# Kernel optimization log

Measured on AMD Instinct MI355X. Metric: run time of the kernel, lower is better.

The kernel has to match this reference:

```python
import jax, jax.numpy as jnp
import numpy as np

H = 64        # hidden_dim
HEADS = 4
HD = H // HEADS

def setup_inputs() -> dict:
    key = jax.random.key(0)
    ks = jax.random.split(key, 32)
    def w(k, shape, fan_in):
        return jax.random.normal(k, shape, dtype=jnp.float32) * (1.0 / np.sqrt(fan_in))
    inp = {
        'robot_states': jax.random.normal(ks[0], (32, 512, 7), dtype=jnp.float32),
        'task_states': jax.random.normal(ks[1], (32, 128, 6), dtype=jnp.float32),
        # robot encoder: Linear(7,H) ReLU Linear(H,H) ReLU
        'r_w1': w(ks[2], (7, H), 7),  'r_b1': jnp.zeros((H,), jnp.float32),
        'r_w2': w(ks[3], (H, H), H),  'r_b2': jnp.zeros((H,), jnp.float32),
        # task encoder: Linear(6,H) ReLU Linear(H,H) ReLU
        't_w1': w(ks[4], (6, H), 6),  't_b1': jnp.zeros((H,), jnp.float32),
        't_w2': w(ks[5], (H, H), H),  't_b2': jnp.zeros((H,), jnp.float32),
        # MultiheadAttention (query=tasks, key/value=robots)
        'wq': w(ks[6], (H, H), H), 'bq': jnp.zeros((H,), jnp.float32),
        'wk': w(ks[7], (H, H), H), 'bk': jnp.zeros((H,), jnp.float32),
        'wv': w(ks[8], (H, H), H), 'bv': jnp.zeros((H,), jnp.float32),
        'wo': w(ks[9], (H, H), H), 'bo': jnp.zeros((H,), jnp.float32),
        # allocation net: Linear(2H,H) ReLU Linear(H,H//2) ReLU Linear(H//2,1)
        'a_w1': w(ks[10], (2 * H, H), 2 * H), 'a_b1': jnp.zeros((H,), jnp.float32),
        'a_w2': w(ks[11], (H, H // 2), H),    'a_b2': jnp.zeros((H // 2,), jnp.float32),
        'a_w3': w(ks[12], (H // 2, 1), H // 2), 'a_b3': jnp.zeros((1,), jnp.float32),
        'num_robots': 512,
        'num_tasks': 128,
    }
    return inp

def reference(robot_states, task_states, r_w1, r_b1, r_w2, r_b2,
              t_w1, t_b1, t_w2, t_b2, wq, bq, wk, bk, wv, bv, wo, bo,
              a_w1, a_b1, a_w2, a_b2, a_w3, a_b3, num_robots, num_tasks):
    relu = jax.nn.relu
    B = robot_states.shape[0]
    # encoders
    rf = relu(relu(robot_states @ r_w1 + r_b1) @ r_w2 + r_b2)[:, :num_robots]  # [B,R,H]
    tf = relu(relu(task_states @ t_w1 + t_b1) @ t_w2 + t_b2)[:, :num_tasks]    # [B,T,H]
    # multihead attention: tasks attend to robots
    q = (tf @ wq + bq).reshape(B, -1, HEADS, HD)
    k = (rf @ wk + bk).reshape(B, -1, HEADS, HD)
    v = (rf @ wv + bv).reshape(B, -1, HEADS, HD)
    logits = jnp.einsum('bthd,brhd->bhtr', q, k) / np.sqrt(HD)
    attn = jax.nn.softmax(logits, axis=-1)
    ctx = jnp.einsum('bhtr,brhd->bthd', attn, v).reshape(B, -1, H)
    tf = ctx @ wo + bo  # [B,T,H]
    # pairwise allocation MLP: concat([task, robot]) @ a_w1 split into two halves
    tp = tf @ a_w1[:H]   # [B,T,H]
    rp = rf @ a_w1[H:]   # [B,R,H]
    h1 = relu(tp[:, :, None, :] + rp[:, None, :, :] + a_b1)  # [B,T,R,H]
    h2 = relu(h1 @ a_w2 + a_b2)                              # [B,T,R,H//2]
    scores = (h2 @ a_w3)[..., 0] + a_b3[0]                   # [B,T,R]
    return jax.nn.softmax(scores, axis=-1)
```

## Files before the change

### kernel.cpp

```cpp
#include <hip/hip_runtime.h>
#include <hip/hip_bf16.h>
#include <math.h>

#define NB 32
#define NR 512
#define NT 128

typedef __attribute__((ext_vector_type(8))) short short8;
typedef __attribute__((ext_vector_type(4))) float f32x4;
typedef __attribute__((ext_vector_type(2))) float f32x2;

#define DPPF(s, ctrl) \
  __int_as_float(__builtin_amdgcn_update_dpp(0, __float_as_int(s), ctrl, 0xf, 0xf, true))

__device__ __forceinline__ float wred_max(float v){
  v = fmaxf(v, DPPF(v, 0xB1));
  v = fmaxf(v, DPPF(v, 0x4E));
  v = fmaxf(v, DPPF(v, 0x141));
  v = fmaxf(v, DPPF(v, 0x140));
  v = fmaxf(v, __shfl_xor(v, 16));
  v = fmaxf(v, __shfl_xor(v, 32));
  return v;
}
__device__ __forceinline__ float wred_sum(float v){
  v += DPPF(v, 0xB1);
  v += DPPF(v, 0x4E);
  v += DPPF(v, 0x141);
  v += DPPF(v, 0x140);
  v += __shfl_xor(v, 16);
  v += __shfl_xor(v, 32);
  return v;
}

__device__ __forceinline__ float dpp_add16(float s){
  int x;
  x = __builtin_amdgcn_update_dpp(0, __float_as_int(s), 0x111, 0xf, 0xf, true);
  s += __int_as_float(x);
  x = __builtin_amdgcn_update_dpp(0, __float_as_int(s), 0x112, 0xf, 0xf, true);
  s += __int_as_float(x);
  x = __builtin_amdgcn_update_dpp(0, __float_as_int(s), 0x114, 0xf, 0xf, true);
  s += __int_as_float(x);
  x = __builtin_amdgcn_update_dpp(0, __float_as_int(s), 0x118, 0xf, 0xf, true);
  s += __int_as_float(x);
  return s;
}

__global__ __launch_bounds__(256) void enc_kernel(
    const float* __restrict__ rs, const float* __restrict__ ts,
    const float* __restrict__ r_w1, const float* __restrict__ r_b1,
    const float* __restrict__ r_w2, const float* __restrict__ r_b2,
    const float* __restrict__ t_w1, const float* __restrict__ t_b1,
    const float* __restrict__ t_w2, const float* __restrict__ t_b2,
    const float* __restrict__ wq, const float* __restrict__ bq,
    const float* __restrict__ wk, const float* __restrict__ bk,
    const float* __restrict__ wv, const float* __restrict__ bv,
    const float* __restrict__ a_w1, const float* __restrict__ a_w2,
    float* __restrict__ kbuf, float* __restrict__ vbuf,
    float* __restrict__ rpbuf, float* __restrict__ qbuf,
    unsigned short* __restrict__ w2f)
{
  __shared__ float w1s[448];
  __shared__ float wss[4096];
  __shared__ float h_s[32 * 66];
  __shared__ float rf_s[32 * 66];

  const int tid = threadIdx.x;
  const int blk = blockIdx.x;

  if (blk == 640) {
    if (tid < 64) {
      int l = tid, n16 = l & 15, g = l >> 4;
      for (int f = 0; f < 8; ++f) {
        int ntile = f & 1, ks = (f >> 1) & 1, part = f >> 2;
        for (int j = 0; j < 8; ++j) {
          int k = ks * 32 + g * 8 + j;
          int n = ntile * 16 + n16;
          unsigned wb = __float_as_uint(a_w2[k * 32 + n]);
          unsigned hib = wb & 0xffff0000u;
          float lof = __uint_as_float(wb) - __uint_as_float(hib);
          unsigned lob = __float_as_uint(lof) & 0xffff0000u;
          w2f[((size_t)f * 64 + l) * 8 + j] =
              (unsigned short)((part == 0 ? hib : lob) >> 16);
        }
      }
    }
    return;
  }

  const int rb = tid >> 3, t8 = tid & 7;
  const bool robot = blk < 512;

  if (robot) {
    if (tid < 112) ((float4*)w1s)[tid] = ((const float4*)r_w1)[tid];
#pragma unroll
    for (int c = 0; c < 4; ++c)
      ((float4*)wss)[c * 256 + tid] = ((const float4*)r_w2)[c * 256 + tid];
  } else {
    if (tid < 96) ((float4*)w1s)[tid] = ((const float4*)t_w1)[tid];
#pragma unroll
    for (int c = 0; c < 4; ++c)
      ((float4*)wss)[c * 256 + tid] = ((const float4*)t_w2)[c * 256 + tid];
  }

  int g, K1;
  const float* xin; const float* b1; const float* b2;
  if (robot) { g = blk * 32 + rb;          K1 = 7; xin = rs + (size_t)g * 7; b1 = r_b1; b2 = r_b2; }
  else       { g = (blk - 512) * 32 + rb;  K1 = 6; xin = ts + (size_t)g * 6; b1 = t_b1; b2 = t_b2; }

  float x[7];
  for (int k = 0; k < K1; ++k) x[k] = xin[k];
  __syncthreads();

  {
    float acc[8];
#pragma unroll
    for (int jj = 0; jj < 8; ++jj) acc[jj] = b1[t8 * 8 + jj];
    for (int k = 0; k < K1; ++k) {
      float xv = x[k];
#pragma unroll
      for (int jj = 0; jj < 8; ++jj) acc[jj] += xv * w1s[k * 64 + t8 * 8 + jj];
    }
#pragma unroll
    for (int jj = 0; jj < 8; ++jj) h_s[rb * 66 + t8 * 8 + jj] = fmaxf(acc[jj], 0.f);
  }
  __syncthreads();

  {
    float acc[8];
#pragma unroll
    for (int jj = 0; jj < 8; ++jj) acc[jj] = b2[t8 * 8 + jj];
    for (int k = 0; k < 64; ++k) {
      float hv = h_s[rb * 66 + k];
      const float4* wr = (const float4*)(wss + k * 64 + t8 * 8);
#pragma unroll
      for (int j4 = 0; j4 < 2; ++j4) {
        float4 w = wr[j4];
        acc[j4 * 4 + 0] += hv * w.x; acc[j4 * 4 + 1] += hv * w.y;
        acc[j4 * 4 + 2] += hv * w.z; acc[j4 * 4 + 3] += hv * w.w;
      }
    }
#pragma unroll
    for (int jj = 0; jj < 8; ++jj) rf_s[rb * 66 + t8 * 8 + jj] = fmaxf(acc[jj], 0.f);
  }

  const float* wp[3]; const float* bp[3]; float* op[3]; int npass;
  if (robot) {
    wp[0] = wk; bp[0] = bk;      op[0] = kbuf;
    wp[1] = wv; bp[1] = bv;      op[1] = vbuf;
    wp[2] = a_w1 + 64 * 64; bp[2] = nullptr; op[2] = rpbuf;
    npass = 3;
  } else {
    wp[0] = wq; bp[0] = bq; op[0] = qbuf; npass = 1;
  }
  for (int p = 0; p < npass; ++p) {
    __syncthreads();
#pragma unroll
    for (int c = 0; c < 4; ++c)
      ((float4*)wss)[c * 256 + tid] = ((const float4*)wp[p])[c * 256 + tid];
    __syncthreads();
    float acc[8];
#pragma unroll
    for (int jj = 0; jj < 8; ++jj) acc[jj] = bp[p] ? bp[p][t8 * 8 + jj] : 0.f;
    for (int k = 0; k < 64; ++k) {
      float hv = rf_s[rb * 66 + k];
      const float4* wr = (const float4*)(wss + k * 64 + t8 * 8);
#pragma unroll
      for (int j4 = 0; j4 < 2; ++j4) {
        float4 w = wr[j4];
        acc[j4 * 4 + 0] += hv * w.x; acc[j4 * 4 + 1] += hv * w.y;
        acc[j4 * 4 + 2] += hv * w.z; acc[j4 * 4 + 3] += hv * w.w;
      }
    }
    float4* o4 = (float4*)(op[p] + (size_t)g * 64 + t8 * 8);
    o4[0] = make_float4(acc[0], acc[1], acc[2], acc[3]);
    o4[1] = make_float4(acc[4], acc[5], acc[6], acc[7]);
  }
}

__device__ __forceinline__ void mk2(f32x2 r, f32x2 t,
                                    unsigned* h, unsigned* l)
{
  f32x2 x = r + t;
  x = __builtin_elementwise_max(x, (f32x2){0.f, 0.f});
  __hip_bfloat162 hb = __float22bfloat162_rn(make_float2(x.x, x.y));
  unsigned hh; __builtin_memcpy(&hh, &hb, 4);
  f32x2 hf;
  hf.x = __int_as_float((int)(hh << 16));
  hf.y = __int_as_float((int)(hh & 0xffff0000u));
  f32x2 e = x - hf;
  __hip_bfloat162 lb = __float22bfloat162_rn(make_float2(e.x, e.y));
  unsigned ll; __builtin_memcpy(&ll, &lb, 4);
  *h = hh; *l = ll;
}

__device__ __forceinline__ void mk_frags(float4 ra, float4 rb,
                                         float4 ta, float4 tb,
                                         short8* Ah, short8* Al)
{
  unsigned h0, h1, h2, h3, l0, l1, l2, l3;
  mk2((f32x2){ra.x, ra.y}, (f32x2){ta.x, ta.y}, &h0, &l0);
  mk2((f32x2){ra.z, ra.w}, (f32x2){ta.z, ta.w}, &h1, &l1);
  mk2((f32x2){rb.x, rb.y}, (f32x2){tb.x, tb.y}, &h2, &l2);
  mk2((f32x2){rb.z, rb.w}, (f32x2){tb.z, tb.w}, &h3, &l3);
  *Ah = __builtin_bit_cast(short8, make_int4((int)h0, (int)h1, (int)h2, (int)h3));
  *Al = __builtin_bit_cast(short8, make_int4((int)l0, (int)l1, (int)l2, (int)l3));
}

#define LGS 520
__global__ __launch_bounds__(256, 4) void attn_pair_kernel(
    const float* __restrict__ qbuf, const float* __restrict__ kbuf,
    const float* __restrict__ vbuf,
    const float* __restrict__ wo, const float* __restrict__ bo,
    const float* __restrict__ a_w1, const float* __restrict__ a_b1,
    const unsigned short* __restrict__ w2f,
    const float* __restrict__ a_b2, const float* __restrict__ a_w3,
    const float* __restrict__ rpbuf,
    float* __restrict__ out)
{
  __shared__ float qt_s[2 * 64];
  __shared__ float lg[2][4 * LGS];
  __shared__ float inv_s[8];
  __shared__ float cp[4][2 * 64];
  __shared__ float ctx_s[2 * 64];
  __shared__ float tp_f[2 * 64];
  __shared__ float red_a[4];
  __shared__ float red_b[4];

  float* const lgf = (float*)lg;

  const int tid = threadIdx.x;
  const int jj = blockIdx.x & 31;
  const int b  = (jj & 7) * 4 + (jj >> 3);
  const int t0 = (blockIdx.x >> 5) * 2;

  if (tid < 32) {
    int tt = tid >> 4, i4 = tid & 15;
    float4 v = ((const float4*)(qbuf + (size_t)(b * NT + t0 + tt) * 64))[i4];
    v.x *= 0.25f; v.y *= 0.25f; v.z *= 0.25f; v.w *= 0.25f;
    ((float4*)qt_s)[tid] = v;
  }
  __syncthreads();

  {
    const int h = tid & 3;
    const int r0 = tid >> 2;
    const f32x4* q0p = (const f32x4*)(qt_s + h * 16);
    const f32x4* q1p = (const f32x4*)(qt_s + 64 + h * 16);
    f32x2 q0[8], q1[8];
#pragma unroll
    for (int j = 0; j < 4; ++j) {
      f32x4 a = q0p[j], c = q1p[j];
      q0[2 * j]     = __builtin_shufflevector(a, a, 0, 1);
      q0[2 * j + 1] = __builtin_shufflevector(a, a, 2, 3);
      q1[2 * j]     = __builtin_shufflevector(c, c, 0, 1);
      q1[2 * j + 1] = __builtin_shufflevector(c, c, 2, 3);
    }
    const float* kb0 = kbuf + (size_t)b * NR * 64 + h * 16;
    for (int it = 0; it < 8; ++it) {
      int r = r0 + it * 64;
      const f32x4* k4 = (const f32x4*)(kb0 + (size_t)r * 64);
      f32x2 a0 = {0.f, 0.f}, a1 = {0.f, 0.f};
#pragma unroll
      for (int j = 0; j < 4; ++j) {
        f32x4 kv = k4[j];
        f32x2 kl = __builtin_shufflevector(kv, kv, 0, 1);
        f32x2 kh = __builtin_shufflevector(kv, kv, 2, 3);
        a0 = __builtin_elementwise_fma(kl, q0[2 * j], a0);
        a0 = __builtin_elementwise_fma(kh, q0[2 * j + 1], a0);
        a1 = __builtin_elementwise_fma(kl, q1[2 * j], a1);
        a1 = __builtin_elementwise_fma(kh, q1[2 * j + 1], a1);
      }
      lg[0][h * LGS + r] = a0.x + a0.y;
      lg[1][h * LGS + r] = a1.x + a1.y;
    }
  }
  __syncthreads();

  {
    int w = tid >> 6, lane = tid & 63;
    for (int p = 0; p < 2; ++p) {
      int pr = w * 2 + p, tt = pr >> 2, hh = pr & 3;
      float* row = &lg[tt][hh * LGS];
      float v0[8];
#pragma unroll
      for (int u = 0; u < 8; ++u) v0[u] = row[u * 64 + lane];
      float m = v0[0];
#pragma unroll
      for (int u = 1; u < 8; ++u) m = fmaxf(m, v0[u]);
      m = wred_max(m);
      float s = 0.f;
#pragma unroll
      for (int u = 0; u < 8; ++u) {
        float e = __expf(v0[u] - m);
        row[u * 64 + lane] = e;
        s += e;
      }
      s = wred_sum(s);
      if (lane == 0) inv_s[tt * 4 + hh] = __builtin_amdgcn_rcpf(s);
    }
  }
  __syncthreads();

  {
    const int dg = tid & 15, rc = tid >> 4;
    const int h = dg >> 2;
    const float* vptr = vbuf + (size_t)b * NR * 64 + dg * 4;
    const float* p0r = &lg[0][h * LGS];
    const float* p1r = &lg[1][h * LGS];
    f32x4 acc0 = {0.f, 0.f, 0.f, 0.f}, acc1 = {0.f, 0.f, 0.f, 0.f};
#pragma unroll 4
    for (int i = 0; i < 32; ++i) {
      int r = rc * 32 + i;
      f32x4 vv = *(const f32x4*)(vptr + (size_t)r * 64);
      float p0 = p0r[r], p1 = p1r[r];
      acc0 = __builtin_elementwise_fma(vv, (f32x4){p0, p0, p0, p0}, acc0);
      acc1 = __builtin_elementwise_fma(vv, (f32x4){p1, p1, p1, p1}, acc1);
    }
    __syncthreads();
    *(f32x4*)(lgf + rc * 132 + dg * 4)      = acc0;
    *(f32x4*)(lgf + rc * 132 + 64 + dg * 4) = acc1;
  }
  __syncthreads();
  if (tid < 128) {
    float s = 0.f;
#pragma unroll
    for (int rc = 0; rc < 16; ++rc) s += lgf[rc * 132 + tid];
    ctx_s[tid] = s * inv_s[(tid >> 6) * 4 + ((tid & 63) >> 4)];
  }
  __syncthreads();

  {
    int jd = tid & 63, kc = tid >> 6;
    float p0 = 0.f, p1 = 0.f;
    for (int k = 0; k < 16; ++k) {
      float w = wo[(kc * 16 + k) * 64 + jd];
      p0 += ctx_s[kc * 16 + k] * w;
      p1 += ctx_s[64 + kc * 16 + k] * w;
    }
    cp[kc][jd]      = p0;
    cp[kc][64 + jd] = p1;
  }
  __syncthreads();
  if (tid < 128) {
    int jd = tid & 63;
    qt_s[tid] = cp[0][tid] + cp[1][tid] + cp[2][tid] + cp[3][tid] + bo[jd];
  }
  __syncthreads();

  {
    int jd = tid & 63, kc = tid >> 6;
    float p0 = 0.f, p1 = 0.f;
    for (int k = 0; k < 16; ++k) {
      float w = a_w1[(kc * 16 + k) * 64 + jd];
      p0 += qt_s[kc * 16 + k] * w;
      p1 += qt_s[64 + kc * 16 + k] * w;
    }
    cp[kc][jd]      = p0;
    cp[kc][64 + jd] = p1;
  }
  __syncthreads();
  if (tid < 128) {
    int jd = tid & 63;
    tp_f[tid] = cp[0][tid] + cp[1][tid] + cp[2][tid] + cp[3][tid] + a_b1[jd];
  }
  __syncthreads();

  const int wave = tid >> 6, lane = tid & 63;
  const int n16 = lane & 15, g = lane >> 4;

  short8 B[8];
#pragma unroll
  for (int f = 0; f < 8; ++f)
    B[f] = __builtin_bit_cast(short8, ((const int4*)w2f)[f * 64 + lane]);

  const float* tpA = tp_f + g * 8;
  const float* tpB = tp_f + 64 + g * 8;
  float4 tA0a = *(const float4*)(tpA),      tA0b = *(const float4*)(tpA + 4);
  float4 tA1a = *(const float4*)(tpA + 32), tA1b = *(const float4*)(tpA + 36);
  float4 tB0a = *(const float4*)(tpB),      tB0b = *(const float4*)(tpB + 4);
  float4 tB1a = *(const float4*)(tpB + 32), tB1b = *(const float4*)(tpB + 36);

  float b20 = a_b2[n16], b21 = a_b2[16 + n16];
  float w30 = a_w3[n16], w31 = a_w3[16 + n16];

  const float* rpb = rpbuf + (size_t)b * NR * 64 + g * 8;

  const float4* rp0 = (const float4*)(rpb + (size_t)(wave * 128 + n16) * 64);
  float4 ra0 = rp0[0], rb0 = rp0[1], ra1 = rp0[8], rb1 = rp0[9];

#pragma unroll
  for (int mt = 0; mt < 8; ++mt) {
    float4 na0, nb0, na1, nb1;
    if (mt < 7) {
      const float4* rpn =
          (const float4*)(rpb + (size_t)(wave * 128 + (mt + 1) * 16 + n16) * 64);
      na0 = rpn[0]; nb0 = rpn[1]; na1 = rpn[8]; nb1 = rpn[9];
    }

#pragma unroll
    for (int task = 0; task < 2; ++task) {
      short8 Ah0, Al0, Ah1, Al1;
      if (task == 0) {
        mk_frags(ra0, rb0, tA0a, tA0b, &Ah0, &Al0);
        mk_frags(ra1, rb1, tA1a, tA1b, &Ah1, &Al1);
      } else {
        mk_frags(ra0, rb0, tB0a, tB0b, &Ah0, &Al0);
        mk_frags(ra1, rb1, tB1a, tB1b, &Ah1, &Al1);
      }
      f32x4 acc0 = (f32x4){b20, b20, b20, b20};
      f32x4 acc1 = (f32x4){b21, b21, b21, b21};
      acc0 = __builtin_amdgcn_mfma_f32_16x16x32_bf16(Ah0, B[0], acc0, 0, 0, 0);
      acc1 = __builtin_amdgcn_mfma_f32_16x16x32_bf16(Ah0, B[1], acc1, 0, 0, 0);
      acc0 = __builtin_amdgcn_mfma_f32_16x16x32_bf16(Al0, B[0], acc0, 0, 0, 0);
      acc1 = __builtin_amdgcn_mfma_f32_16x16x32_bf16(Al0, B[1], acc1, 0, 0, 0);
      acc0 = __builtin_amdgcn_mfma_f32_16x16x32_bf16(Ah0, B[4], acc0, 0, 0, 0);
      acc1 = __builtin_amdgcn_mfma_f32_16x16x32_bf16(Ah0, B[5], acc1, 0, 0, 0);
      acc0 = __builtin_amdgcn_mfma_f32_16x16x32_bf16(Ah1, B[2], acc0, 0, 0, 0);
      acc1 = __builtin_amdgcn_mfma_f32_16x16x32_bf16(Ah1, B[3], acc1, 0, 0, 0);
      acc0 = __builtin_amdgcn_mfma_f32_16x16x32_bf16(Al1, B[2], acc0, 0, 0, 0);
      acc1 = __builtin_amdgcn_mfma_f32_16x16x32_bf16(Al1, B[3], acc1, 0, 0, 0);
      acc0 = __builtin_amdgcn_mfma_f32_16x16x32_bf16(Ah1, B[6], acc0, 0, 0, 0);
      acc1 = __builtin_amdgcn_mfma_f32_16x16x32_bf16(Ah1, B[7], acc1, 0, 0, 0);
#pragma unroll
      for (int reg = 0; reg < 4; ++reg) {
        float s = fmaxf(acc0[reg], 0.f) * w30 + fmaxf(acc1[reg], 0.f) * w31;
        s = dpp_add16(s);
        if (n16 == 15)
          lgf[task * 512 + wave * 128 + mt * 16 + g * 4 + reg] = s;
      }
    }
    ra0 = na0; rb0 = nb0; ra1 = na1; rb1 = nb1;
  }
  __syncthreads();

  const int lw = tid & 63, wid = tid >> 6;
  for (int task = 0; task < 2; ++task) {
    float s0 = lgf[task * 512 + tid], s1 = lgf[task * 512 + tid + 256];
    float mw = wred_max(fmaxf(s0, s1));
    if (lw == 0) red_a[wid] = mw;
    __syncthreads();
    float m = fmaxf(fmaxf(red_a[0], red_a[1]), fmaxf(red_a[2], red_a[3]));
    float e0 = __expf(s0 - m), e1 = __expf(s1 - m);
    float sw = wred_sum(e0 + e1);
    if (lw == 0) red_b[wid] = sw;
    __syncthreads();
    float inv = __builtin_amdgcn_rcpf(red_b[0] + red_b[1] + red_b[2] + red_b[3]);
    float* op = out + (size_t)(b * NT + t0 + task) * NR;
    op[tid]       = e0 * inv;
    op[256 + tid] = e1 * inv;
  }
}

extern "C" void kernel_launch(void* const* d_in, const int* in_sizes, int n_in,
                              void* d_out, int out_size, void* d_ws, size_t ws_size,
                              hipStream_t stream)
{
  const float* rs   = (const float*)d_in[0];
  const float* ts   = (const float*)d_in[1];
  const float* r_w1 = (const float*)d_in[2];  const float* r_b1 = (const float*)d_in[3];
  const float* r_w2 = (const float*)d_in[4];  const float* r_b2 = (const float*)d_in[5];
  const float* t_w1 = (const float*)d_in[6];  const float* t_b1 = (const float*)d_in[7];
  const float* t_w2 = (const float*)d_in[8];  const float* t_b2 = (const float*)d_in[9];
  const float* wq   = (const float*)d_in[10]; const float* bq   = (const float*)d_in[11];
  const float* wk   = (const float*)d_in[12]; const float* bk   = (const float*)d_in[13];
  const float* wv   = (const float*)d_in[14]; const float* bv   = (const float*)d_in[15];
  const float* wo   = (const float*)d_in[16]; const float* bo   = (const float*)d_in[17];
  const float* a_w1 = (const float*)d_in[18]; const float* a_b1 = (const float*)d_in[19];
  const float* a_w2 = (const float*)d_in[20]; const float* a_b2 = (const float*)d_in[21];
  const float* a_w3 = (const float*)d_in[22]; const float* a_b3 = (const float*)d_in[23];

  float* wsf   = (float*)d_ws;
  float* kbuf  = wsf;
  float* vbuf  = kbuf  + (size_t)NB * NR * 64;
  float* rpbuf = vbuf  + (size_t)NB * NR * 64;
  float* qbuf  = rpbuf + (size_t)NB * NR * 64;
  unsigned short* w2f = (unsigned short*)(qbuf + (size_t)NB * NT * 64);

  enc_kernel<<<dim3(641), dim3(256), 0, stream>>>(
      rs, ts, r_w1, r_b1, r_w2, r_b2, t_w1, t_b1, t_w2, t_b2,
      wq, bq, wk, bk, wv, bv, a_w1, a_w2, kbuf, vbuf, rpbuf, qbuf, w2f);

  attn_pair_kernel<<<dim3(2048), dim3(256), 0, stream>>>(
      qbuf, kbuf, vbuf, wo, bo, a_w1, a_b1, w2f, a_b2, a_w3, rpbuf,
      (float*)d_out);
}
```

Before: 196.6 us.

## Fold wo into a_w1 and restructure attention to per-wave heads with register softmax

Precomputes the fused weight wo@a_w1[:H] and the bias bo@a_w1[:H]+a_b1 once in the spare encoder block. This removes one 64x64 projection stage and two block barriers from every attention block. The attention phase now gives each wave one head, keeps logits and the softmax in registers, and writes only the probabilities to shared memory. The P·V partial sums are reduced with ds_swizzle and shuffles instead of a shared-memory pass. The trade-off is extra serial work in the single encoder block, and float rounding changes slightly because of the reassociated matmul.

```diff
diff --git a/kernel.cpp b/kernel.cpp
--- a/kernel.cpp
+++ b/kernel.cpp
@@ -45,6 +45,14 @@
   return s;
 }
 
+#define SWZ4(acc, OFF) \
+  do { \
+    _Pragma("unroll") \
+    for (int _i = 0; _i < 4; ++_i) \
+      acc[_i] += __int_as_float(__builtin_amdgcn_ds_swizzle( \
+          __float_as_int(acc[_i]), OFF)); \
+  } while (0)
+
 __global__ __launch_bounds__(256) void enc_kernel(
     const float* __restrict__ rs, const float* __restrict__ ts,
     const float* __restrict__ r_w1, const float* __restrict__ r_b1,
@@ -55,9 +63,12 @@
     const float* __restrict__ wk, const float* __restrict__ bk,
     const float* __restrict__ wv, const float* __restrict__ bv,
     const float* __restrict__ a_w1, const float* __restrict__ a_w2,
+    const float* __restrict__ wo, const float* __restrict__ bo,
+    const float* __restrict__ a_b1,
     float* __restrict__ kbuf, float* __restrict__ vbuf,
     float* __restrict__ rpbuf, float* __restrict__ qbuf,
-    unsigned short* __restrict__ w2f)
+    unsigned short* __restrict__ w2f,
+    float* __restrict__ wfuse, float* __restrict__ bfuse)
 {
   __shared__ float w1s[448];
   __shared__ float wss[4096];
@@ -68,6 +79,10 @@
   const int blk = blockIdx.x;
 
   if (blk == 640) {
+#pragma unroll
+    for (int c = 0; c < 4; ++c)
+      ((float4*)wss)[c * 256 + tid] = ((const float4*)wo)[c * 256 + tid];
+
     if (tid < 64) {
       int l = tid, n16 = l & 15, g = l >> 4;
       for (int f = 0; f < 8; ++f) {
@@ -84,6 +99,28 @@
         }
       }
     }
+    __syncthreads();
+
+    {
+      const int j = tid & 63, kg = tid >> 6;
+      float acc[16];
+#pragma unroll
+      for (int kk = 0; kk < 16; ++kk) acc[kk] = 0.f;
+      for (int m = 0; m < 64; ++m) {
+        float aw = a_w1[m * 64 + j];
+#pragma unroll
+        for (int kk = 0; kk < 16; ++kk)
+          acc[kk] += wss[(kg * 16 + kk) * 64 + m] * aw;
+      }
+#pragma unroll
+      for (int kk = 0; kk < 16; ++kk)
+        wfuse[(kg * 16 + kk) * 64 + j] = acc[kk];
+    }
+    if (tid < 64) {
+      float acc = a_b1[tid];
+      for (int m = 0; m < 64; ++m) acc += bo[m] * a_w1[m * 64 + tid];
+      bfuse[tid] = acc;
+    }
     return;
   }
 
@@ -206,59 +243,53 @@
   *Al = __builtin_bit_cast(short8, make_int4((int)l0, (int)l1, (int)l2, (int)l3));
 }
 
-#define LGS 520
 __global__ __launch_bounds__(256, 4) void attn_pair_kernel(
     const float* __restrict__ qbuf, const float* __restrict__ kbuf,
     const float* __restrict__ vbuf,
-    const float* __restrict__ wo, const float* __restrict__ bo,
-    const float* __restrict__ a_w1, const float* __restrict__ a_b1,
+    const float* __restrict__ wfuse, const float* __restrict__ bfuse,
     const unsigned short* __restrict__ w2f,
     const float* __restrict__ a_b2, const float* __restrict__ a_w3,
     const float* __restrict__ rpbuf,
     float* __restrict__ out)
 {
-  __shared__ float qt_s[2 * 64];
-  __shared__ float lg[2][4 * LGS];
-  __shared__ float inv_s[8];
+  __shared__ float p_s[4 * 1056];
   __shared__ float cp[4][2 * 64];
   __shared__ float ctx_s[2 * 64];
   __shared__ float tp_f[2 * 64];
   __shared__ float red_a[4];
   __shared__ float red_b[4];
 
-  float* const lgf = (float*)lg;
+  float* const lgf = p_s;
 
   const int tid = threadIdx.x;
   const int jj = blockIdx.x & 31;
   const int b  = (jj & 7) * 4 + (jj >> 3);
   const int t0 = (blockIdx.x >> 5) * 2;
 
-  if (tid < 32) {
-    int tt = tid >> 4, i4 = tid & 15;
-    float4 v = ((const float4*)(qbuf + (size_t)(b * NT + t0 + tt) * 64))[i4];
-    v.x *= 0.25f; v.y *= 0.25f; v.z *= 0.25f; v.w *= 0.25f;
-    ((float4*)qt_s)[tid] = v;
-  }
-  __syncthreads();
+  const int wave = tid >> 6, lane = tid & 63;
+  const int h = wave;
 
   {
-    const int h = tid & 3;
-    const int r0 = tid >> 2;
-    const f32x4* q0p = (const f32x4*)(qt_s + h * 16);
-    const f32x4* q1p = (const f32x4*)(qt_s + 64 + h * 16);
     f32x2 q0[8], q1[8];
-#pragma unroll
-    for (int j = 0; j < 4; ++j) {
-      f32x4 a = q0p[j], c = q1p[j];
-      q0[2 * j]     = __builtin_shufflevector(a, a, 0, 1);
-      q0[2 * j + 1] = __builtin_shufflevector(a, a, 2, 3);
-      q1[2 * j]     = __builtin_shufflevector(c, c, 0, 1);
-      q1[2 * j + 1] = __builtin_shufflevector(c, c, 2, 3);
-    }
+    {
+      const f32x4* qp0 = (const f32x4*)(qbuf + (size_t)(b * NT + t0) * 64 + h * 16);
+      const f32x4* qp1 = (const f32x4*)(qbuf + (size_t)(b * NT + t0 + 1) * 64 + h * 16);
+#pragma unroll
+      for (int j = 0; j < 4; ++j) {
+        f32x4 a = qp0[j] * 0.25f;
+        f32x4 c = qp1[j] * 0.25f;
+        q0[2 * j]     = __builtin_shufflevector(a, a, 0, 1);
+        q0[2 * j + 1] = __builtin_shufflevector(a, a, 2, 3);
+        q1[2 * j]     = __builtin_shufflevector(c, c, 0, 1);
+        q1[2 * j + 1] = __builtin_shufflevector(c, c, 2, 3);
+      }
+    }
+
+    float e0[8], e1[8];
     const float* kb0 = kbuf + (size_t)b * NR * 64 + h * 16;
-    for (int it = 0; it < 8; ++it) {
-      int r = r0 + it * 64;
-      const f32x4* k4 = (const f32x4*)(kb0 + (size_t)r * 64);
+#pragma unroll
+    for (int u = 0; u < 8; ++u) {
+      const f32x4* k4 = (const f32x4*)(kb0 + (size_t)(lane + u * 64) * 64);
       f32x2 a0 = {0.f, 0.f}, a1 = {0.f, 0.f};
 #pragma unroll
       for (int j = 0; j < 4; ++j) {
@@ -270,62 +301,57 @@
         a1 = __builtin_elementwise_fma(kl, q1[2 * j], a1);
         a1 = __builtin_elementwise_fma(kh, q1[2 * j + 1], a1);
       }
-      lg[0][h * LGS + r] = a0.x + a0.y;
-      lg[1][h * LGS + r] = a1.x + a1.y;
-    }
-  }
-  __syncthreads();
-
-  {
-    int w = tid >> 6, lane = tid & 63;
-    for (int p = 0; p < 2; ++p) {
-      int pr = w * 2 + p, tt = pr >> 2, hh = pr & 3;
-      float* row = &lg[tt][hh * LGS];
-      float v0[8];
-#pragma unroll
-      for (int u = 0; u < 8; ++u) v0[u] = row[u * 64 + lane];
-      float m = v0[0];
-#pragma unroll
-      for (int u = 1; u < 8; ++u) m = fmaxf(m, v0[u]);
-      m = wred_max(m);
-      float s = 0.f;
-#pragma unroll
-      for (int u = 0; u < 8; ++u) {
-        float e = __expf(v0[u] - m);
-        row[u * 64 + lane] = e;
-        s += e;
-      }
-      s = wred_sum(s);
-      if (lane == 0) inv_s[tt * 4 + hh] = __builtin_amdgcn_rcpf(s);
-    }
-  }
-  __syncthreads();
-
-  {
-    const int dg = tid & 15, rc = tid >> 4;
-    const int h = dg >> 2;
-    const float* vptr = vbuf + (size_t)b * NR * 64 + dg * 4;
-    const float* p0r = &lg[0][h * LGS];
-    const float* p1r = &lg[1][h * LGS];
-    f32x4 acc0 = {0.f, 0.f, 0.f, 0.f}, acc1 = {0.f, 0.f, 0.f, 0.f};
-#pragma unroll 4
-    for (int i = 0; i < 32; ++i) {
-      int r = rc * 32 + i;
-      f32x4 vv = *(const f32x4*)(vptr + (size_t)r * 64);
-      float p0 = p0r[r], p1 = p1r[r];
-      acc0 = __builtin_elementwise_fma(vv, (f32x4){p0, p0, p0, p0}, acc0);
-      acc1 = __builtin_elementwise_fma(vv, (f32x4){p1, p1, p1, p1}, acc1);
-    }
-    __syncthreads();
-    *(f32x4*)(lgf + rc * 132 + dg * 4)      = acc0;
-    *(f32x4*)(lgf + rc * 132 + 64 + dg * 4) = acc1;
-  }
-  __syncthreads();
-  if (tid < 128) {
-    float s = 0.f;
-#pragma unroll
-    for (int rc = 0; rc < 16; ++rc) s += lgf[rc * 132 + tid];
-    ctx_s[tid] = s * inv_s[(tid >> 6) * 4 + ((tid & 63) >> 4)];
+      e0[u] = a0.x + a0.y;
+      e1[u] = a1.x + a1.y;
+    }
+
+    float m0 = e0[0], m1 = e1[0];
+#pragma unroll
+    for (int u = 1; u < 8; ++u) { m0 = fmaxf(m0, e0[u]); m1 = fmaxf(m1, e1[u]); }
+    m0 = wred_max(m0);  m1 = wred_max(m1);
+    float s0 = 0.f, s1 = 0.f;
+#pragma unroll
+    for (int u = 0; u < 8; ++u) {
+      e0[u] = __expf(e0[u] - m0);  s0 += e0[u];
+      e1[u] = __expf(e1[u] - m1);  s1 += e1[u];
+    }
+    s0 = wred_sum(s0);  s1 = wred_sum(s1);
+    float inv0 = __builtin_amdgcn_rcpf(s0);
+    float inv1 = __builtin_amdgcn_rcpf(s1);
+
+    {
+      float* pw = p_s + h * 1056 + (lane >> 5) * 66 + (lane & 31) * 2;
+#pragma unroll
+      for (int u = 0; u < 8; ++u)
+        *(f32x2*)(pw + u * 132) = (f32x2){e0[u], e1[u]};
+    }
+
+    {
+      const int dq = lane & 3, c = lane >> 2;
+      const float* vp = vbuf + (size_t)b * NR * 64 + (size_t)c * 32 * 64 + h * 16 + dq * 4;
+      const float* pr = p_s + h * 1056 + c * 66;
+      f32x4 acc0 = {0.f, 0.f, 0.f, 0.f}, acc1 = {0.f, 0.f, 0.f, 0.f};
+#pragma unroll 8
+      for (int i = 0; i < 32; ++i) {
+        f32x4 vv = *(const f32x4*)(vp + (size_t)i * 64);
+        f32x2 p2 = *(const f32x2*)(pr + i * 2);
+        acc0 = __builtin_elementwise_fma(vv, (f32x4){p2.x, p2.x, p2.x, p2.x}, acc0);
+        acc1 = __builtin_elementwise_fma(vv, (f32x4){p2.y, p2.y, p2.y, p2.y}, acc1);
+      }
+      SWZ4(acc0, 0x101F); SWZ4(acc1, 0x101F);
+      SWZ4(acc0, 0x201F); SWZ4(acc1, 0x201F);
+      SWZ4(acc0, 0x401F); SWZ4(acc1, 0x401F);
+#pragma unroll
+      for (int i = 0; i < 4; ++i) {
+        acc0[i] += __shfl_xor(acc0[i], 32);
+        acc1[i] += __shfl_xor(acc1[i], 32);
+      }
+      acc0 *= inv0;  acc1 *= inv1;
+      if (lane < 4) {
+        *(f32x4*)(ctx_s + h * 16 + lane * 4)      = acc0;
+        *(f32x4*)(ctx_s + 64 + h * 16 + lane * 4) = acc1;
+      }
+    }
   }
   __syncthreads();
 
@@ -333,7 +359,7 @@
     int jd = tid & 63, kc = tid >> 6;
     float p0 = 0.f, p1 = 0.f;
     for (int k = 0; k < 16; ++k) {
-      float w = wo[(kc * 16 + k) * 64 + jd];
+      float w = wfuse[(kc * 16 + k) * 64 + jd];
       p0 += ctx_s[kc * 16 + k] * w;
       p1 += ctx_s[64 + kc * 16 + k] * w;
     }
@@ -343,29 +369,10 @@
   __syncthreads();
   if (tid < 128) {
     int jd = tid & 63;
-    qt_s[tid] = cp[0][tid] + cp[1][tid] + cp[2][tid] + cp[3][tid] + bo[jd];
-  }
-  __syncthreads();
-
-  {
-    int jd = tid & 63, kc = tid >> 6;
-    float p0 = 0.f, p1 = 0.f;
-    for (int k = 0; k < 16; ++k) {
-      float w = a_w1[(kc * 16 + k) * 64 + jd];
-      p0 += qt_s[kc * 16 + k] * w;
-      p1 += qt_s[64 + kc * 16 + k] * w;
-    }
-    cp[kc][jd]      = p0;
-    cp[kc][64 + jd] = p1;
-  }
-  __syncthreads();
-  if (tid < 128) {
-    int jd = tid & 63;
-    tp_f[tid] = cp[0][tid] + cp[1][tid] + cp[2][tid] + cp[3][tid] + a_b1[jd];
-  }
-  __syncthreads();
-
-  const int wave = tid >> 6, lane = tid & 63;
+    tp_f[tid] = cp[0][tid] + cp[1][tid] + cp[2][tid] + cp[3][tid] + bfuse[jd];
+  }
+  __syncthreads();
+
   const int n16 = lane & 15, g = lane >> 4;
 
   short8 B[8];
@@ -475,12 +482,15 @@
   float* rpbuf = vbuf  + (size_t)NB * NR * 64;
   float* qbuf  = rpbuf + (size_t)NB * NR * 64;
   unsigned short* w2f = (unsigned short*)(qbuf + (size_t)NB * NT * 64);
+  float* wfuse = (float*)(w2f + 8 * 64 * 8);
+  float* bfuse = wfuse + 64 * 64;
 
   enc_kernel<<<dim3(641), dim3(256), 0, stream>>>(
       rs, ts, r_w1, r_b1, r_w2, r_b2, t_w1, t_b1, t_w2, t_b2,
-      wq, bq, wk, bk, wv, bv, a_w1, a_w2, kbuf, vbuf, rpbuf, qbuf, w2f);
+      wq, bq, wk, bk, wv, bv, a_w1, a_w2, wo, bo, a_b1,
+      kbuf, vbuf, rpbuf, qbuf, w2f, wfuse, bfuse);
 
   attn_pair_kernel<<<dim3(2048), dim3(256), 0, stream>>>(
-      qbuf, kbuf, vbuf, wo, bo, a_w1, a_b1, w2f, a_b2, a_w3, rpbuf,
+      qbuf, kbuf, vbuf, wfuse, bfuse, w2f, a_b2, a_w3, rpbuf,
       (float*)d_out);
 }
```

Result: slower. 221.5 us (+12.7%).

## Fold out-proj into allocation weights and transpose pair MFMA to drop DPP reduction

Applied to the files above, without the earlier changes.

Precomputes wo@a_w1[:H] and bo@a_w1[:H]+a_b1 once in the spare encoder block, which removes one 64x64 matvec stage and two barriers per attention block. Swaps the MFMA operands so each lane holds four hidden units of one pair. The a_w3 dot then becomes an in-register FMA chain, and the 16-lane DPP reduction and masked stores are replaced by four partial writes that get summed at softmax time. The softmax is also restructured so both tasks are processed at once with fewer barriers. The cost is a larger logits buffer in LDS, plus added serial work in the single precompute block of the encoder kernel.

```diff
diff --git a/kernel.cpp b/kernel.cpp
--- a/kernel.cpp
+++ b/kernel.cpp
@@ -30,19 +30,6 @@
   v += __shfl_xor(v, 16);
   v += __shfl_xor(v, 32);
   return v;
-}
-
-__device__ __forceinline__ float dpp_add16(float s){
-  int x;
-  x = __builtin_amdgcn_update_dpp(0, __float_as_int(s), 0x111, 0xf, 0xf, true);
-  s += __int_as_float(x);
-  x = __builtin_amdgcn_update_dpp(0, __float_as_int(s), 0x112, 0xf, 0xf, true);
-  s += __int_as_float(x);
-  x = __builtin_amdgcn_update_dpp(0, __float_as_int(s), 0x114, 0xf, 0xf, true);
-  s += __int_as_float(x);
-  x = __builtin_amdgcn_update_dpp(0, __float_as_int(s), 0x118, 0xf, 0xf, true);
-  s += __int_as_float(x);
-  return s;
 }
 
 __global__ __launch_bounds__(256) void enc_kernel(
@@ -55,9 +42,12 @@
     const float* __restrict__ wk, const float* __restrict__ bk,
     const float* __restrict__ wv, const float* __restrict__ bv,
     const float* __restrict__ a_w1, const float* __restrict__ a_w2,
+    const float* __restrict__ wo, const float* __restrict__ bo,
+    const float* __restrict__ a_b1,
     float* __restrict__ kbuf, float* __restrict__ vbuf,
     float* __restrict__ rpbuf, float* __restrict__ qbuf,
-    unsigned short* __restrict__ w2f)
+    unsigned short* __restrict__ w2f,
+    float* __restrict__ wfuse, float* __restrict__ bfuse)
 {
   __shared__ float w1s[448];
   __shared__ float wss[4096];
@@ -68,6 +58,10 @@
   const int blk = blockIdx.x;
 
   if (blk == 640) {
+#pragma unroll
+    for (int c = 0; c < 4; ++c)
+      ((float4*)wss)[c * 256 + tid] = ((const float4*)wo)[c * 256 + tid];
+
     if (tid < 64) {
       int l = tid, n16 = l & 15, g = l >> 4;
       for (int f = 0; f < 8; ++f) {
@@ -84,6 +78,28 @@
         }
       }
     }
+    __syncthreads();
+
+    {
+      const int j = tid & 63, kg = tid >> 6;
+      float acc[16];
+#pragma unroll
+      for (int kk = 0; kk < 16; ++kk) acc[kk] = 0.f;
+      for (int m = 0; m < 64; ++m) {
+        float aw = a_w1[m * 64 + j];
+#pragma unroll
+        for (int kk = 0; kk < 16; ++kk)
+          acc[kk] += wss[(kg * 16 + kk) * 64 + m] * aw;
+      }
+#pragma unroll
+      for (int kk = 0; kk < 16; ++kk)
+        wfuse[(kg * 16 + kk) * 64 + j] = acc[kk];
+    }
+    if (tid < 64) {
+      float acc = a_b1[tid];
+      for (int m = 0; m < 64; ++m) acc += bo[m] * a_w1[m * 64 + tid];
+      bfuse[tid] = acc;
+    }
     return;
   }
 
@@ -210,8 +226,7 @@
 __global__ __launch_bounds__(256, 4) void attn_pair_kernel(
     const float* __restrict__ qbuf, const float* __restrict__ kbuf,
     const float* __restrict__ vbuf,
-    const float* __restrict__ wo, const float* __restrict__ bo,
-    const float* __restrict__ a_w1, const float* __restrict__ a_b1,
+    const float* __restrict__ wfuse, const float* __restrict__ bfuse,
     const unsigned short* __restrict__ w2f,
     const float* __restrict__ a_b2, const float* __restrict__ a_w3,
     const float* __restrict__ rpbuf,
@@ -333,7 +348,7 @@
     int jd = tid & 63, kc = tid >> 6;
     float p0 = 0.f, p1 = 0.f;
     for (int k = 0; k < 16; ++k) {
-      float w = wo[(kc * 16 + k) * 64 + jd];
+      float w = wfuse[(kc * 16 + k) * 64 + jd];
       p0 += ctx_s[kc * 16 + k] * w;
       p1 += ctx_s[64 + kc * 16 + k] * w;
     }
@@ -343,35 +358,18 @@
   __syncthreads();
   if (tid < 128) {
     int jd = tid & 63;
-    qt_s[tid] = cp[0][tid] + cp[1][tid] + cp[2][tid] + cp[3][tid] + bo[jd];
-  }
-  __syncthreads();
-
-  {
-    int jd = tid & 63, kc = tid >> 6;
-    float p0 = 0.f, p1 = 0.f;
-    for (int k = 0; k < 16; ++k) {
-      float w = a_w1[(kc * 16 + k) * 64 + jd];
-      p0 += qt_s[kc * 16 + k] * w;
-      p1 += qt_s[64 + kc * 16 + k] * w;
-    }
-    cp[kc][jd]      = p0;
-    cp[kc][64 + jd] = p1;
-  }
-  __syncthreads();
-  if (tid < 128) {
-    int jd = tid & 63;
-    tp_f[tid] = cp[0][tid] + cp[1][tid] + cp[2][tid] + cp[3][tid] + a_b1[jd];
+    tp_f[tid] = cp[0][tid] + cp[1][tid] + cp[2][tid] + cp[3][tid] + bfuse[jd];
   }
   __syncthreads();
 
   const int wave = tid >> 6, lane = tid & 63;
   const int n16 = lane & 15, g = lane >> 4;
-
-  short8 B[8];
+  const int d0 = g * 4;
+
+  short8 W[8];
 #pragma unroll
   for (int f = 0; f < 8; ++f)
-    B[f] = __builtin_bit_cast(short8, ((const int4*)w2f)[f * 64 + lane]);
+    W[f] = __builtin_bit_cast(short8, ((const int4*)w2f)[f * 64 + lane]);
 
   const float* tpA = tp_f + g * 8;
   const float* tpB = tp_f + 64 + g * 8;
@@ -380,8 +378,10 @@
   float4 tB0a = *(const float4*)(tpB),      tB0b = *(const float4*)(tpB + 4);
   float4 tB1a = *(const float4*)(tpB + 32), tB1b = *(const float4*)(tpB + 36);
 
-  float b20 = a_b2[n16], b21 = a_b2[16 + n16];
-  float w30 = a_w3[n16], w31 = a_w3[16 + n16];
+  f32x4 bias0 = *(const f32x4*)(a_b2 + d0);
+  f32x4 bias1 = *(const f32x4*)(a_b2 + 16 + d0);
+  f32x4 w3v0  = *(const f32x4*)(a_w3 + d0);
+  f32x4 w3v1  = *(const f32x4*)(a_w3 + 16 + d0);
 
   const float* rpb = rpbuf + (size_t)b * NR * 64 + g * 8;
 
@@ -399,55 +399,67 @@
 
 #pragma unroll
     for (int task = 0; task < 2; ++task) {
-      short8 Ah0, Al0, Ah1, Al1;
+      short8 Hh0, Hl0, Hh1, Hl1;
       if (task == 0) {
-        mk_frags(ra0, rb0, tA0a, tA0b, &Ah0, &Al0);
-        mk_frags(ra1, rb1, tA1a, tA1b, &Ah1, &Al1);
+        mk_frags(ra0, rb0, tA0a, tA0b, &Hh0, &Hl0);
+        mk_frags(ra1, rb1, tA1a, tA1b, &Hh1, &Hl1);
       } else {
-        mk_frags(ra0, rb0, tB0a, tB0b, &Ah0, &Al0);
-        mk_frags(ra1, rb1, tB1a, tB1b, &Ah1, &Al1);
-      }
-      f32x4 acc0 = (f32x4){b20, b20, b20, b20};
-      f32x4 acc1 = (f32x4){b21, b21, b21, b21};
-      acc0 = __builtin_amdgcn_mfma_f32_16x16x32_bf16(Ah0, B[0], acc0, 0, 0, 0);
-      acc1 = __builtin_amdgcn_mfma_f32_16x16x32_bf16(Ah0, B[1], acc1, 0, 0, 0);
-      acc0 = __builtin_amdgcn_mfma_f32_16x16x32_bf16(Al0, B[0], acc0, 0, 0, 0);
-      acc1 = __builtin_amdgcn_mfma_f32_16x16x32_bf16(Al0, B[1], acc1, 0, 0, 0);
-      acc0 = __builtin_amdgcn_mfma_f32_16x16x32_bf16(Ah0, B[4], acc0, 0, 0, 0);
-      acc1 = __builtin_amdgcn_mfma_f32_16x16x32_bf16(Ah0, B[5], acc1, 0, 0, 0);
-      acc0 = __builtin_amdgcn_mfma_f32_16x16x32_bf16(Ah1, B[2], acc0, 0, 0, 0);
-      acc1 = __builtin_amdgcn_mfma_f32_16x16x32_bf16(Ah1, B[3], acc1, 0, 0, 0);
-      acc0 = __builtin_amdgcn_mfma_f32_16x16x32_bf16(Al1, B[2], acc0, 0, 0, 0);
-      acc1 = __builtin_amdgcn_mfma_f32_16x16x32_bf16(Al1, B[3], acc1, 0, 0, 0);
-      acc0 = __builtin_amdgcn_mfma_f32_16x16x32_bf16(Ah1, B[6], acc0, 0, 0, 0);
-      acc1 = __builtin_amdgcn_mfma_f32_16x16x32_bf16(Ah1, B[7], acc1, 0, 0, 0);
-#pragma unroll
-      for (int reg = 0; reg < 4; ++reg) {
-        float s = fmaxf(acc0[reg], 0.f) * w30 + fmaxf(acc1[reg], 0.f) * w31;
-        s = dpp_add16(s);
-        if (n16 == 15)
-          lgf[task * 512 + wave * 128 + mt * 16 + g * 4 + reg] = s;
-      }
+        mk_frags(ra0, rb0, tB0a, tB0b, &Hh0, &Hl0);
+        mk_frags(ra1, rb1, tB1a, tB1b, &Hh1, &Hl1);
+      }
+      f32x4 acc0 = bias0;
+      f32x4 acc1 = bias1;
+      acc0 = __builtin_amdgcn_mfma_f32_16x16x32_bf16(W[0], Hh0, acc0, 0, 0, 0);
+      acc1 = __builtin_amdgcn_mfma_f32_16x16x32_bf16(W[1], Hh0, acc1, 0, 0, 0);
+      acc0 = __builtin_amdgcn_mfma_f32_16x16x32_bf16(W[0], Hl0, acc0, 0, 0, 0);
+      acc1 = __builtin_amdgcn_mfma_f32_16x16x32_bf16(W[1], Hl0, acc1, 0, 0, 0);
+      acc0 = __builtin_amdgcn_mfma_f32_16x16x32_bf16(W[4], Hh0, acc0, 0, 0, 0);
+      acc1 = __builtin_amdgcn_mfma_f32_16x16x32_bf16(W[5], Hh0, acc1, 0, 0, 0);
+      acc0 = __builtin_amdgcn_mfma_f32_16x16x32_bf16(W[2], Hh1, acc0, 0, 0, 0);
+      acc1 = __builtin_amdgcn_mfma_f32_16x16x32_bf16(W[3], Hh1, acc1, 0, 0, 0);
+      acc0 = __builtin_amdgcn_mfma_f32_16x16x32_bf16(W[2], Hl1, acc0, 0, 0, 0);
+      acc1 = __builtin_amdgcn_mfma_f32_16x16x32_bf16(W[3], Hl1, acc1, 0, 0, 0);
+      acc0 = __builtin_amdgcn_mfma_f32_16x16x32_bf16(W[6], Hh1, acc0, 0, 0, 0);
+      acc1 = __builtin_amdgcn_mfma_f32_16x16x32_bf16(W[7], Hh1, acc1, 0, 0, 0);
+      float s =           fmaxf(acc0[0], 0.f) * w3v0[0];
+      s = fmaf(fmaxf(acc0[1], 0.f), w3v0[1], s);
+      s = fmaf(fmaxf(acc0[2], 0.f), w3v0[2], s);
+      s = fmaf(fmaxf(acc0[3], 0.f), w3v0[3], s);
+      s = fmaf(fmaxf(acc1[0], 0.f), w3v1[0], s);
+      s = fmaf(fmaxf(acc1[1], 0.f), w3v1[1], s);
+      s = fmaf(fmaxf(acc1[2], 0.f), w3v1[2], s);
+      s = fmaf(fmaxf(acc1[3], 0.f), w3v1[3], s);
+      lgf[task * 2048 + g * 512 + wave * 128 + mt * 16 + n16] = s;
     }
     ra0 = na0; rb0 = nb0; ra1 = na1; rb1 = nb1;
   }
   __syncthreads();
 
-  const int lw = tid & 63, wid = tid >> 6;
-  for (int task = 0; task < 2; ++task) {
-    float s0 = lgf[task * 512 + tid], s1 = lgf[task * 512 + tid + 256];
-    float mw = wred_max(fmaxf(s0, s1));
-    if (lw == 0) red_a[wid] = mw;
+  {
+    const int task = tid >> 7, t2 = tid & 127;
+    const int lw = tid & 63, wid = tid >> 6;
+    const float* pp = lgf + task * 2048;
+    float v[4];
+#pragma unroll
+    for (int u = 0; u < 4; ++u) {
+      int r = t2 + u * 128;
+      v[u] = (pp[r] + pp[512 + r]) + (pp[1024 + r] + pp[1536 + r]);
+    }
+    float m = fmaxf(fmaxf(v[0], v[1]), fmaxf(v[2], v[3]));
+    m = wred_max(m);
+    if (lw == 0) red_a[wid] = m;
     __syncthreads();
-    float m = fmaxf(fmaxf(red_a[0], red_a[1]), fmaxf(red_a[2], red_a[3]));
-    float e0 = __expf(s0 - m), e1 = __expf(s1 - m);
-    float sw = wred_sum(e0 + e1);
-    if (lw == 0) red_b[wid] = sw;
+    m = fmaxf(red_a[task * 2], red_a[task * 2 + 1]);
+    float e[4], ss = 0.f;
+#pragma unroll
+    for (int u = 0; u < 4; ++u) { e[u] = __expf(v[u] - m); ss += e[u]; }
+    ss = wred_sum(ss);
+    if (lw == 0) red_b[wid] = ss;
     __syncthreads();
-    float inv = __builtin_amdgcn_rcpf(red_b[0] + red_b[1] + red_b[2] + red_b[3]);
+    float inv = __builtin_amdgcn_rcpf(red_b[task * 2] + red_b[task * 2 + 1]);
     float* op = out + (size_t)(b * NT + t0 + task) * NR;
-    op[tid]       = e0 * inv;
-    op[256 + tid] = e1 * inv;
+#pragma unroll
+    for (int u = 0; u < 4; ++u) op[t2 + u * 128] = e[u] * inv;
   }
 }
 
@@ -475,12 +487,15 @@
   float* rpbuf = vbuf  + (size_t)NB * NR * 64;
   float* qbuf  = rpbuf + (size_t)NB * NR * 64;
   unsigned short* w2f = (unsigned short*)(qbuf + (size_t)NB * NT * 64);
+  float* wfuse = (float*)(w2f + 8 * 64 * 8);
+  float* bfuse = wfuse + 64 * 64;
 
   enc_kernel<<<dim3(641), dim3(256), 0, stream>>>(
       rs, ts, r_w1, r_b1, r_w2, r_b2, t_w1, t_b1, t_w2, t_b2,
-      wq, bq, wk, bk, wv, bv, a_w1, a_w2, kbuf, vbuf, rpbuf, qbuf, w2f);
+      wq, bq, wk, bk, wv, bv, a_w1, a_w2, wo, bo, a_b1,
+      kbuf, vbuf, rpbuf, qbuf, w2f, wfuse, bfuse);
 
   attn_pair_kernel<<<dim3(2048), dim3(256), 0, stream>>>(
-      qbuf, kbuf, vbuf, wo, bo, a_w1, a_b1, w2f, a_b2, a_w3, rpbuf,
+      qbuf, kbuf, vbuf, wfuse, bfuse, w2f, a_b2, a_w3, rpbuf,
       (float*)d_out);
 }
```

Result: slower. 261.9 us (+33.2%).
